# Kernel tuning notes

Hardware: AMD Instinct MI355X
Metric: run time of the kernel (lower is better)

The kernel has to match this reference:

```python
import jax, jax.numpy as jnp
import numpy as np

N_EXPERTS = 8
D = 4096
B = 16


def setup_inputs() -> dict:
    key = jax.random.key(0)
    kx, kw, ki = jax.random.split(key, 3)
    x = jax.random.normal(kx, (B, 1, D), dtype=jnp.float32)
    W = jax.random.normal(kw, (N_EXPERTS, D, D), dtype=jnp.float32) * 0.02
    indices = jax.random.randint(ki, (B,), 0, N_EXPERTS, dtype=jnp.int64)
    return {"x": x, "indices": indices, "W": W}


def reference(x, indices, W):
    # indices wrapped into [0, 8) as in the torch module
    idx = indices.astype(jnp.int32) % N_EXPERTS
    # Gather per-sample expert weight: (B, D, D). The original materializes
    # this tensor explicitly via torch.gather; we do the equivalent take.
    Wg = W[idx]                                   # (B, D, D)
    # x: (B, 1, D) -> x_expanded: (B, 1, 1, D); gathered squeeze is a no-op,
    # so matmul broadcasts over the extra singleton dim -> (B, 1, 1, D).
    out = jnp.einsum('bod,bde->boe', x, Wg)       # (B, 1, D)
    return out[:, None]                           # (B, 1, 1, D) as torch returns
```

## Files before the change

kernel.cpp:

```cpp
#include <hip/hip_runtime.h>
#include <hip/hip_bf16.h>


#define NEXP 8
#define BATCH 16
#define DIM 4096
#define SPB 8
#define CHUNKS_PER_E 2
#define COLS_PER_BLOCK 1024
#define COL_TILES (DIM / COLS_PER_BLOCK)
#define KCH 128
#define K_CHUNKS (DIM / KCH)

__global__ void group_kernel(const void* __restrict__ idx_raw,
                             int* __restrict__ counts,
                             int* __restrict__ lists) {
    if (threadIdx.x != 0 || blockIdx.x != 0) return;
    const long long* i64 = (const long long*)idx_raw;
    const int*       i32 = (const int*)idx_raw;
    bool is64 = true;
    for (int k = 0; k < 8; ++k) {
        long long v = i64[k];
        if (v < 0 || v >= NEXP) { is64 = false; break; }
    }
    int cnt[NEXP];
    for (int e = 0; e < NEXP; ++e) cnt[e] = 0;
    for (int b = 0; b < BATCH; ++b) {
        long long vi = is64 ? i64[b] : (long long)i32[b];
        int e = (int)(((vi % NEXP) + NEXP) % NEXP);
        lists[e * BATCH + cnt[e]] = b;
        cnt[e]++;
    }
    for (int e = 0; e < NEXP; ++e) counts[e] = cnt[e];
}

__global__ __launch_bounds__(256)
void gmm_kernel(const float* __restrict__ x,
                const float* __restrict__ W,
                const int* __restrict__ counts,
                const int* __restrict__ lists,
                float* __restrict__ out) {
    const int ez    = blockIdx.z;
    const int e     = ez >> 1;
    const int chunk = ez & 1;
    const int c_e   = counts[e];
    const int base_s = chunk * SPB;
    if (base_s >= c_e) return;
    const int nvalid = min(SPB, c_e - base_s);

    __shared__ float xs[SPB][KCH];
    __shared__ int   samp[SPB];

    const int tid   = threadIdx.x;
    const int krow0 = blockIdx.y * KCH;

    if (tid < SPB) {
        const int slot = base_s + tid;
        samp[tid] = (tid < nvalid) ? lists[e * BATCH + slot] : -1;
    }
    __syncthreads();

    for (int i = tid; i < SPB * KCH; i += 256) {
        const int s = i >> 7;
        const int d = i & (KCH - 1);
        const int sm = samp[s];
        xs[s][d] = (sm >= 0) ? x[(size_t)sm * DIM + krow0 + d] : 0.0f;
    }
    __syncthreads();

    const int col0 = blockIdx.x * COLS_PER_BLOCK + tid * 4;
    const float4* Wp = (const float4*)(W + (size_t)e * DIM * DIM
                                        + (size_t)krow0 * DIM + col0);

    float4 acc[SPB];
#pragma unroll
    for (int s = 0; s < SPB; ++s) acc[s] = make_float4(0.f, 0.f, 0.f, 0.f);

#pragma unroll 4
    for (int d = 0; d < KCH; ++d) {
        const float4 w = Wp[(size_t)d * (DIM / 4)];
#pragma unroll
        for (int s = 0; s < SPB; ++s) {
            const float xv = xs[s][d];
            acc[s].x = fmaf(xv, w.x, acc[s].x);
            acc[s].y = fmaf(xv, w.y, acc[s].y);
            acc[s].z = fmaf(xv, w.z, acc[s].z);
            acc[s].w = fmaf(xv, w.w, acc[s].w);
        }
    }

#pragma unroll
    for (int s = 0; s < SPB; ++s) {
        const int sm = samp[s];
        if (sm >= 0) {
            float* o = out + (size_t)sm * DIM + col0;
            atomicAdd(o + 0, acc[s].x);
            atomicAdd(o + 1, acc[s].y);
            atomicAdd(o + 2, acc[s].z);
            atomicAdd(o + 3, acc[s].w);
        }
    }
}

extern "C" void kernel_launch(void* const* d_in, const int* in_sizes, int n_in,
                              void* d_out, int out_size, void* d_ws, size_t ws_size,
                              hipStream_t stream) {
    const float* x   = (const float*)d_in[0];
    const void*  idx = d_in[1];
    const float* W   = (const float*)d_in[2];
    float* out = (float*)d_out;

    int* counts = (int*)d_ws;
    int* lists  = counts + NEXP;

    hipMemsetAsync(d_out, 0, (size_t)out_size * sizeof(float), stream);

    group_kernel<<<1, 64, 0, stream>>>(idx, counts, lists);

    dim3 grid(COL_TILES, K_CHUNKS, NEXP * CHUNKS_PER_E);
    gmm_kernel<<<grid, 256, 0, stream>>>(x, W, counts, lists, out);
}
```

Baseline: 692.6 us.

## Fuse expert grouping into GEMV kernel and specialize inner loop on sample count

Removes the separate single-thread grouping kernel: each block's thread 0 now scans the indices itself to find its samples. The x tile in shared memory is transposed to [k][sample] so the per-k sample values are contiguous. The inner FMA loop is templated on 2, 4 or 8 active samples to skip work for sparsely used experts. The unroll factor is raised to 8. This saves a kernel launch and a serial dependency, at the cost of redundant index scanning in every block.

```diff
diff --git a/kernel.cpp b/kernel.cpp
--- a/kernel.cpp
+++ b/kernel.cpp
@@ -1,97 +1,95 @@
 #include <hip/hip_runtime.h>
-#include <hip/hip_bf16.h>
 
 
 #define NEXP 8
 #define BATCH 16
 #define DIM 4096
 #define SPB 8
-#define CHUNKS_PER_E 2
 #define COLS_PER_BLOCK 1024
 #define COL_TILES (DIM / COLS_PER_BLOCK)
 #define KCH 128
 #define K_CHUNKS (DIM / KCH)
 
-__global__ void group_kernel(const void* __restrict__ idx_raw,
-                             int* __restrict__ counts,
-                             int* __restrict__ lists) {
-    if (threadIdx.x != 0 || blockIdx.x != 0) return;
-    const long long* i64 = (const long long*)idx_raw;
-    const int*       i32 = (const int*)idx_raw;
-    bool is64 = true;
-    for (int k = 0; k < 8; ++k) {
-        long long v = i64[k];
-        if (v < 0 || v >= NEXP) { is64 = false; break; }
-    }
-    int cnt[NEXP];
-    for (int e = 0; e < NEXP; ++e) cnt[e] = 0;
-    for (int b = 0; b < BATCH; ++b) {
-        long long vi = is64 ? i64[b] : (long long)i32[b];
-        int e = (int)(((vi % NEXP) + NEXP) % NEXP);
-        lists[e * BATCH + cnt[e]] = b;
-        cnt[e]++;
-    }
-    for (int e = 0; e < NEXP; ++e) counts[e] = cnt[e];
-}
-
-__global__ __launch_bounds__(256)
-void gmm_kernel(const float* __restrict__ x,
-                const float* __restrict__ W,
-                const int* __restrict__ counts,
-                const int* __restrict__ lists,
-                float* __restrict__ out) {
-    const int ez    = blockIdx.z;
-    const int e     = ez >> 1;
-    const int chunk = ez & 1;
-    const int c_e   = counts[e];
-    const int base_s = chunk * SPB;
-    if (base_s >= c_e) return;
-    const int nvalid = min(SPB, c_e - base_s);
-
-    __shared__ float xs[SPB][KCH];
-    __shared__ int   samp[SPB];
-
-    const int tid   = threadIdx.x;
-    const int krow0 = blockIdx.y * KCH;
-
-    if (tid < SPB) {
-        const int slot = base_s + tid;
-        samp[tid] = (tid < nvalid) ? lists[e * BATCH + slot] : -1;
-    }
-    __syncthreads();
-
-    for (int i = tid; i < SPB * KCH; i += 256) {
-        const int s = i >> 7;
-        const int d = i & (KCH - 1);
-        const int sm = samp[s];
-        xs[s][d] = (sm >= 0) ? x[(size_t)sm * DIM + krow0 + d] : 0.0f;
-    }
-    __syncthreads();
-
-    const int col0 = blockIdx.x * COLS_PER_BLOCK + tid * 4;
-    const float4* Wp = (const float4*)(W + (size_t)e * DIM * DIM
-                                        + (size_t)krow0 * DIM + col0);
-
-    float4 acc[SPB];
-#pragma unroll
-    for (int s = 0; s < SPB; ++s) acc[s] = make_float4(0.f, 0.f, 0.f, 0.f);
-
-#pragma unroll 4
+template<int S>
+__device__ __forceinline__ void inner_loop(const float4* __restrict__ Wp,
+                                           const float (* __restrict__ xs)[SPB],
+                                           float4* __restrict__ acc) {
+#pragma unroll 8
     for (int d = 0; d < KCH; ++d) {
         const float4 w = Wp[(size_t)d * (DIM / 4)];
 #pragma unroll
-        for (int s = 0; s < SPB; ++s) {
-            const float xv = xs[s][d];
+        for (int s = 0; s < S; ++s) {
+            const float xv = xs[d][s];
             acc[s].x = fmaf(xv, w.x, acc[s].x);
             acc[s].y = fmaf(xv, w.y, acc[s].y);
             acc[s].z = fmaf(xv, w.z, acc[s].z);
             acc[s].w = fmaf(xv, w.w, acc[s].w);
         }
     }
+}
+
+__global__ __launch_bounds__(256)
+void gmm_kernel(const float* __restrict__ x,
+                const void* __restrict__ idx_raw,
+                const float* __restrict__ W,
+                float* __restrict__ out) {
+    __shared__ int   s_samp[SPB];
+    __shared__ int   s_nv;
+    __shared__ float xs[KCH][SPB];
+
+    const int tid   = threadIdx.x;
+    const int e     = blockIdx.z >> 1;
+    const int chunk = blockIdx.z & 1;
+
+    if (tid == 0) {
+        const long long* i64 = (const long long*)idx_raw;
+        const int*       i32 = (const int*)idx_raw;
+        bool is64 = true;
+        for (int k = 0; k < 8; ++k) {
+            const long long v = i64[k];
+            if (v < 0 || v >= NEXP) { is64 = false; break; }
+        }
+        const int base = chunk * SPB;
+        int cnt = 0, got = 0;
+        for (int b = 0; b < BATCH; ++b) {
+            const long long vi = is64 ? i64[b] : (long long)i32[b];
+            const int eb = (int)(((vi % NEXP) + NEXP) % NEXP);
+            if (eb == e) {
+                if (cnt >= base && got < SPB) s_samp[got++] = b;
+                cnt++;
+            }
+        }
+        for (int s2 = got; s2 < SPB; ++s2) s_samp[s2] = -1;
+        s_nv = got;
+    }
+    __syncthreads();
+    const int nv = s_nv;
+    if (nv == 0) return;
+
+    const int krow0 = blockIdx.y * KCH;
+
+    for (int i = tid; i < KCH * SPB; i += 256) {
+        const int d = i >> 3, s = i & 7;
+        const int sm = s_samp[s];
+        xs[d][s] = (sm >= 0) ? x[(size_t)sm * DIM + krow0 + d] : 0.f;
+    }
+    __syncthreads();
+
+    const int col0 = blockIdx.x * COLS_PER_BLOCK + tid * 4;
+    const float4* Wp = (const float4*)(W + (size_t)e * DIM * DIM
+                                         + (size_t)krow0 * DIM + col0);
+
+    float4 acc[SPB];
+#pragma unroll
+    for (int s = 0; s < SPB; ++s) acc[s] = make_float4(0.f, 0.f, 0.f, 0.f);
+
+    if (nv <= 2)      inner_loop<2>(Wp, xs, acc);
+    else if (nv <= 4) inner_loop<4>(Wp, xs, acc);
+    else              inner_loop<8>(Wp, xs, acc);
 
 #pragma unroll
     for (int s = 0; s < SPB; ++s) {
-        const int sm = samp[s];
+        const int sm = s_samp[s];
         if (sm >= 0) {
             float* o = out + (size_t)sm * DIM + col0;
             atomicAdd(o + 0, acc[s].x);
@@ -110,13 +108,8 @@
     const float* W   = (const float*)d_in[2];
     float* out = (float*)d_out;
 
-    int* counts = (int*)d_ws;
-    int* lists  = counts + NEXP;
-
     hipMemsetAsync(d_out, 0, (size_t)out_size * sizeof(float), stream);
 
-    group_kernel<<<1, 64, 0, stream>>>(idx, counts, lists);
-
-    dim3 grid(COL_TILES, K_CHUNKS, NEXP * CHUNKS_PER_E);
-    gmm_kernel<<<grid, 256, 0, stream>>>(x, W, counts, lists, out);
+    dim3 grid(COL_TILES, K_CHUNKS, NEXP * 2);
+    gmm_kernel<<<grid, 256, 0, stream>>>(x, idx, W, out);
 }
```

New measurement: 676.8 us. 1.02x faster.
